# Kernel optimization log

Measured on AMD Instinct MI355X. Metric: run time of the kernel, lower is better.

Reference implementation:

```python
import jax, jax.numpy as jnp
import numpy as np

A0, A1, A2 = 1.0, 1.0, 0.5  # Taylor coefficients of exp around 0 (p=2)

B, H, N, D = 2, 16, 4096, 32


def setup_inputs() -> dict:
    key = jax.random.key(0)
    kq, kk, kv = jax.random.split(key, 3)
    q = jax.random.normal(kq, (B, H, N, D), dtype=jnp.float32)
    k = jax.random.normal(kk, (B, H, N, D), dtype=jnp.float32)
    v = jax.random.normal(kv, (B, H, N, D), dtype=jnp.float32)
    return {"q": q, "k": k, "v": v}


def reference(q, k, v):
    # fastmax_function with p=2, mask=False, normalize=False, dropout=0 -> temperature=1
    b, h, n, d = q.shape
    # quadratic feature maps: flatten of outer products, [b,h,n,d*d]
    q2 = (q[..., :, None] * q[..., None, :]).reshape(b, h, n, d * d)
    k2 = (k[..., :, None] * k[..., None, :]).reshape(b, h, n, d * d)
    # numerator: a0*sum(v) + a1*q(k^T v) + a2*q2(k2^T v)
    second_term = A1 * jnp.einsum('bhnd,bhne->bhde', k, v)           # [b,h,d,d]
    third_term = A2 * jnp.einsum('bhnf,bhne->bhfe', k2, v)           # [b,h,d^2,d]
    ans = (jnp.einsum('bhnd,bhde->bhne', q, second_term)
           + jnp.einsum('bhnf,bhfe->bhne', q2, third_term)
           + A0 * jnp.sum(v, axis=-2, keepdims=True))                 # [b,h,n,d]
    # denominator: a0*n + a1*q.sum(k) + a2*q2.sum(k2)
    div = (A0 * n
           + A1 * jnp.einsum('bhnd,bhd->bhn', q, jnp.sum(k, axis=-2))
           + A2 * jnp.einsum('bhnf,bhf->bhn', q2, jnp.sum(k2, axis=-2)))  # [b,h,n]
    return ans / div[..., None]
```

## Files before the change

kernel.cpp:

```cpp
#include <hip/hip_runtime.h>

#define NTOK 4096
#define NBH  32
#define NF   576
#define NE   33
#define NKT  18
#define GTF_BH (NKT * 3 * 64 * 8)
#define KC   16
#define NSTG 2
#define NVB  (KC * NBH)
#define NP8  (NBH * NE * NF / 8)

typedef _Float16 half_t;
typedef _Float16 half8 __attribute__((ext_vector_type(8)));
typedef _Float16 half4v __attribute__((ext_vector_type(4)));
typedef float f32x4 __attribute__((ext_vector_type(4)));

#define MFMA16(A,B,C) __builtin_amdgcn_mfma_f32_16x16x32_f16((A),(B),(C),0,0,0)

static __device__ __forceinline__ half8 splat8(half_t x) {
    return (half8){x, x, x, x, x, x, x, x};
}

static __device__ __forceinline__ int FS(int d) { return (d + (d >> 3)) & 15; }

__global__ __launch_bounds__(256, 2)
void ta_kernel(const float* __restrict__ kin, const float* __restrict__ vin,
               half_t* __restrict__ P)
{
    __shared__ __align__(16) half_t kb0[2 * 4096];
    __shared__ __align__(16) half_t vb0[2 * 4096];

    const int vb = blockIdx.x;
    const int bh = vb & (NBH - 1), kc = vb >> 5;
    const int t = threadIdx.x;
    const int w = t >> 6, lane = t & 63, l16 = lane & 15, quad = lane >> 4;
    const int pw = w * 144;
    const half8 h05 = splat8((half_t)0.5f);

    f32x4 acc[9][3];
    #pragma unroll
    for (int m = 0; m < 9; ++m)
        #pragma unroll
        for (int e = 0; e < 3; ++e)
            acc[m][e] = (f32x4){0.f, 0.f, 0.f, 0.f};

    int rotoff[9], rotsalt[9];
    #pragma unroll
    for (int mt = 0; mt < 9; ++mt) {
        const int pm = pw + mt * 16;
        int ro = 0, rs = 0;
        if (pm >= 32 && pm < 512) {
            const int s  = 1 + ((pm - 32) >> 5);
            const int i0 = (pm - 32) & 31;
            const int r  = (i0 + l16 + s) & 31;
            ro = r * 128;
            rs = FS(r);
        }
        rotoff[mt] = ro;
        rotsalt[mt] = rs;
    }
    const int sh0 = FS(l16), sh1 = FS(l16 + 16);

    const size_t fbase = ((size_t)bh * NTOK + kc * 256) * 32;
    const float4* k4 = (const float4*)kin + fbase / 4;
    const float4* v4 = (const float4*)vin + fbase / 4;

    float kaf[16], vaf[16];
    auto loadst = [&](int s) {
        const int base = s * 1024;
        #pragma unroll
        for (int r = 0; r < 4; ++r) {
            float4 kk = k4[base + t + 256 * r];
            float4 vv = v4[base + t + 256 * r];
            kaf[4*r+0] = kk.x; kaf[4*r+1] = kk.y; kaf[4*r+2] = kk.z; kaf[4*r+3] = kk.w;
            vaf[4*r+0] = vv.x; vaf[4*r+1] = vv.y; vaf[4*r+2] = vv.z; vaf[4*r+3] = vv.w;
        }
    };
    auto writest = [&](int buf) {
        half_t* kb = kb0 + buf * 4096;
        half_t* vb2 = vb0 + buf * 4096;
        #pragma unroll
        for (int r = 0; r < 4; ++r) {
            const int fi = t + 256 * r;
            const int n = fi >> 3, d4 = fi & 7;
            const int c = n >> 3, j = n & 7;
            #pragma unroll
            for (int i = 0; i < 4; ++i) {
                const int d = 4 * d4 + i;
                const int a = d * 128 + ((c ^ FS(d)) << 3) + j;
                kb[a] = (half_t)kaf[4*r+i];
                vb2[a] = (half_t)vaf[4*r+i];
            }
        }
    };
    auto compute = [&](int buf) {
        const half_t* kb = kb0 + buf * 4096;
        const half_t* vbp = vb0 + buf * 4096;
        #pragma unroll
        for (int kk = 0; kk < 4; ++kk) {
            const int c = kk * 4 + quad;
            half8 kj0 = *(const half8*)&kb[l16 * 128 + ((c ^ sh0) << 3)];
            half8 kj1 = *(const half8*)&kb[(l16 + 16) * 128 + ((c ^ sh1) << 3)];
            half8 bf0 = *(const half8*)&vbp[l16 * 128 + ((c ^ sh0) << 3)];
            half8 bf1 = *(const half8*)&vbp[(l16 + 16) * 128 + ((c ^ sh1) << 3)];
            half_t onec = (l16 == 0) ? (half_t)1 : (half_t)0;
            half8 bf2 = splat8(onec);
            #pragma unroll
            for (int mt = 0; mt < 9; ++mt) {
                const int pm = pw + mt * 16;
                half8 af;
                if (pm < 32) {
                    af = pm ? kj1 : kj0;
                } else if (pm < 512) {
                    half8 rot = *(const half8*)&kb[rotoff[mt] + ((c ^ rotsalt[mt]) << 3)];
                    af = (((pm - 32) & 16) ? kj1 : kj0) * rot;
                } else if (pm == 512) {
                    af = kj0 * kj1;
                } else if (pm == 528) {
                    af = (kj0 * h05) * kj0;
                } else if (pm == 544) {
                    af = (kj1 * h05) * kj1;
                } else {
                    af = bf2;
                }
                acc[mt][0] = MFMA16(af, bf0, acc[mt][0]);
                acc[mt][1] = MFMA16(af, bf1, acc[mt][1]);
                acc[mt][2] = MFMA16(af, bf2, acc[mt][2]);
            }
        }
    };

    loadst(0);
    writest(0);
    __syncthreads();
    for (int st = 0; st < NSTG; ++st) {
        const int cur = st & 1;
        if (st + 1 < NSTG) loadst(st + 1);
        compute(cur);
        if (st + 1 < NSTG) { writest(cur ^ 1); __syncthreads(); }
    }

    half_t* Pb = P + ((size_t)kc * NBH + bh) * NE * NF;
    #pragma unroll
    for (int mt = 0; mt < 9; ++mt) {
        int p0 = pw + mt * 16 + quad * 4;
        half4v h0 = {(half_t)acc[mt][0][0], (half_t)acc[mt][0][1],
                     (half_t)acc[mt][0][2], (half_t)acc[mt][0][3]};
        half4v h1 = {(half_t)acc[mt][1][0], (half_t)acc[mt][1][1],
                     (half_t)acc[mt][1][2], (half_t)acc[mt][1][3]};
        *(half4v*)&Pb[(size_t)l16 * NF + p0] = h0;
        *(half4v*)&Pb[(size_t)(l16 + 16) * NF + p0] = h1;
        if (l16 == 0) {
            half4v h2 = {(half_t)acc[mt][2][0], (half_t)acc[mt][2][1],
                         (half_t)acc[mt][2][2], (half_t)acc[mt][2][3]};
            *(half4v*)&Pb[(size_t)32 * NF + p0] = h2;
        }
    }
}

__global__ __launch_bounds__(256)
void ar_kernel(const half_t* __restrict__ P, half_t* __restrict__ GtF)
{
    const int idx = blockIdx.x * 256 + threadIdx.x;
    if (idx >= NP8) return;
    float s[8] = {0.f, 0.f, 0.f, 0.f, 0.f, 0.f, 0.f, 0.f};
    for (int c = 0; c < KC; ++c) {
        half8 h = *(const half8*)&P[(size_t)c * (NBH * NE * NF) + (size_t)idx * 8];
        #pragma unroll
        for (int j = 0; j < 8; ++j) s[j] += (float)h[j];
    }
    half8 o;
    #pragma unroll
    for (int j = 0; j < 8; ++j) o[j] = (half_t)s[j];
    int row = idx / 72;
    int p8 = idx - row * 72;
    int e = row % 33, bhh = row / 33;
    int kt = p8 >> 2, quad = p8 & 3;
    int rr = e >> 4, l16 = e & 15;
    size_t dst8 = (size_t)bhh * (GTF_BH / 8)
                + (size_t)(kt * 3 + rr) * 64 + quad * 16 + l16;
    *(half8*)&GtF[dst8 * 8] = o;
}

__global__ __launch_bounds__(256)
void b_kernel(const float* __restrict__ qin, const half_t* __restrict__ GtF,
              float* __restrict__ out)
{
    const int bh = blockIdx.x, mbq = blockIdx.y;
    const int t = threadIdx.x, w = t >> 6, lane = t & 63;
    const int l16 = lane & 15, quad = lane >> 4;
    __shared__ __align__(16) half_t qs2[256 * 56];
    __shared__ float denl[256];
    const size_t nbase = (size_t)bh * NTOK + mbq * 256;

    const float4* q4 = (const float4*)(qin + nbase * 32);
    #pragma unroll
    for (int r = 0; r < 8; ++r) {
        int f4 = t + 256 * r, n = f4 >> 3, d4 = f4 & 7;
        float4 vv = q4[f4];
        half4v h = {(half_t)vv.x, (half_t)vv.y, (half_t)vv.z, (half_t)vv.w};
        *(half4v*)&qs2[n * 56 + d4 * 4] = h;
        if (d4 < 4) *(half4v*)&qs2[n * 56 + 32 + d4 * 4] = h;
    }
    __syncthreads();

    const int rbase = w * 64;
    int tb[4];
    #pragma unroll
    for (int mt = 0; mt < 4; ++mt) tb[mt] = (rbase + mt * 16 + l16) * 56;

    half8 vq[4], hv[4], gv[4];
    #pragma unroll
    for (int mt = 0; mt < 4; ++mt) {
        const int qb = tb[mt] + quad * 8;
        vq[mt] = *(const half8*)&qs2[qb];
        hv[mt] = *(const half8*)&qs2[qb + 8];
        gv[mt] = *(const half8*)&qs2[qb + 16];
    }

    f32x4 acc[3][4];
    #pragma unroll
    for (int a = 0; a < 3; ++a)
        #pragma unroll
        for (int b = 0; b < 4; ++b)
            acc[a][b] = (f32x4){0.f, 0.f, 0.f, 0.f};

    const half_t* Gb = GtF + (size_t)bh * GTF_BH + (size_t)lane * 8;

#define LDF(kt, B) do { \
    _Pragma("unroll") \
    for (int rr = 0; rr < 3; ++rr) \
        (B)[rr] = *(const half8*)&Gb[(size_t)(((kt) * 3 + rr) * 64) * 8]; \
} while (0)

#define DO_MFMA(AF) do { \
    _Pragma("unroll") \
    for (int mt = 0; mt < 4; ++mt) { \
        acc[0][mt] = MFMA16((AF)[mt], B0[0], acc[0][mt]); \
        acc[1][mt] = MFMA16((AF)[mt], B0[1], acc[1][mt]); \
        acc[2][mt] = MFMA16((AF)[mt], B0[2], acc[2][mt]); \
    } \
} while (0)

#define RING() do { \
    _Pragma("unroll") \
    for (int rr = 0; rr < 3; ++rr) { B0[rr] = B1[rr]; B1[rr] = B2[rr]; B2[rr] = B3[rr]; } \
} while (0)

    half8 B0[3], B1[3], B2[3], B3[3];
    LDF(0, B0); LDF(1, B1); LDF(2, B2);

    {
        LDF(3, B3);
        DO_MFMA(vq);
        RING();
    }

#define QCHUNK(S) do { \
    if ((S) + 3 <= 17) LDF((S) + 3, B3); \
    half8 af[4]; \
    _Pragma("unroll") \
    for (int mt = 0; mt < 4; ++mt) { \
        half8 lo = ((S) < 8) ? vq[mt] : hv[mt]; \
        half8 hi = ((S) < 8) ? hv[mt] : gv[mt]; \
        half8 rot = __builtin_shufflevector(lo, hi, \
            ((S) & 7) + 0, ((S) & 7) + 1, ((S) & 7) + 2, ((S) & 7) + 3, \
            ((S) & 7) + 4, ((S) & 7) + 5, ((S) & 7) + 6, ((S) & 7) + 7); \
        af[mt] = vq[mt] * rot; \
    } \
    DO_MFMA(af); \
    RING(); \
} while (0)

    QCHUNK(1);  QCHUNK(2);  QCHUNK(3);  QCHUNK(4);  QCHUNK(5);
    QCHUNK(6);  QCHUNK(7);  QCHUNK(8);  QCHUNK(9);  QCHUNK(10);
    QCHUNK(11); QCHUNK(12); QCHUNK(13); QCHUNK(14); QCHUNK(15);

    {
        half8 af[4];
        #pragma unroll
        for (int mt = 0; mt < 4; ++mt) {
            const int off = tb[mt] + ((quad >= 2) ? (quad - 2) : quad) * 8;
            half8 Ld = *(const half8*)&qs2[off];
            af[mt] = (quad < 2) ? (vq[mt] * gv[mt]) : (Ld * Ld);
        }
        DO_MFMA(af);
        RING();
    }
    {
        const half8 zero = {};
        half8 c10 = {};
        c10[0] = (half_t)1;
        half8 af[4];
        #pragma unroll
        for (int mt = 0; mt < 4; ++mt) {
            half8 d = gv[mt] * gv[mt];
            af[mt] = (quad < 2) ? d : ((quad == 2) ? c10 : zero);
        }
        DO_MFMA(af);
    }
#undef QCHUNK
#undef RING
#undef DO_MFMA
#undef LDF

    if (l16 == 0) {
        #pragma unroll
        for (int mt = 0; mt < 4; ++mt)
            #pragma unroll
            for (int r = 0; r < 4; ++r)
                denl[rbase + mt * 16 + quad * 4 + r] = acc[2][mt][r];
    }
    __syncthreads();
    #pragma unroll
    for (int mt = 0; mt < 4; ++mt) {
        float inv[4];
        #pragma unroll
        for (int r = 0; r < 4; ++r)
            inv[r] = __builtin_amdgcn_rcpf(denl[rbase + mt * 16 + quad * 4 + r]);
        #pragma unroll
        for (int r = 0; r < 4; ++r) {
            size_t ro = (nbase + rbase + mt * 16 + quad * 4 + r) * 32;
            out[ro + l16] = acc[0][mt][r] * inv[r];
            out[ro + l16 + 16] = acc[1][mt][r] * inv[r];
        }
    }
}

extern "C" void kernel_launch(void* const* d_in, const int* in_sizes, int n_in,
                              void* d_out, int out_size, void* d_ws, size_t ws_size,
                              hipStream_t stream)
{
    const float* q = (const float*)d_in[0];
    const float* k = (const float*)d_in[1];
    const float* v = (const float*)d_in[2];
    float* out = (float*)d_out;

    const size_t planeHalves = (size_t)NBH * NE * NF;
    half_t* P = (half_t*)d_ws;
    half_t* GtF = P + (size_t)KC * planeHalves;

    ta_kernel<<<dim3(NVB), 256, 0, stream>>>(k, v, P);
    ar_kernel<<<dim3((NP8 + 255) / 256), 256, 0, stream>>>(P, GtF);
    b_kernel<<<dim3(NBH, 16), 256, 0, stream>>>(q, GtF, out);
}
```

Before: 123.1 us.

## Replace split-K partial buffer and reduction kernel with fp32 atomics into G

The ta_kernel now accumulates its per-chunk partial products directly into an fp32 G buffer in the b_kernel layout using unsafeAtomicAdd, after a memset. This removes the separate ar_kernel and the fp16 partial plane round trip. b_kernel loads fp32 values and converts them to fp16 on the fly. In exchange it issues many scalar atomics (16-way contention per element), doubles the G read size in b_kernel, and adds a memset launch.

```diff
diff --git a/kernel.cpp b/kernel.cpp
--- a/kernel.cpp
+++ b/kernel.cpp
@@ -9,11 +9,9 @@
 #define KC   16
 #define NSTG 2
 #define NVB  (KC * NBH)
-#define NP8  (NBH * NE * NF / 8)
 
 typedef _Float16 half_t;
 typedef _Float16 half8 __attribute__((ext_vector_type(8)));
-typedef _Float16 half4v __attribute__((ext_vector_type(4)));
 typedef float f32x4 __attribute__((ext_vector_type(4)));
 
 #define MFMA16(A,B,C) __builtin_amdgcn_mfma_f32_16x16x32_f16((A),(B),(C),0,0,0)
@@ -26,7 +24,7 @@
 
 __global__ __launch_bounds__(256, 2)
 void ta_kernel(const float* __restrict__ kin, const float* __restrict__ vin,
-               half_t* __restrict__ P)
+               float* __restrict__ G32)
 {
     __shared__ __align__(16) half_t kb0[2 * 4096];
     __shared__ __align__(16) half_t vb0[2 * 4096];
@@ -141,50 +139,35 @@
         if (st + 1 < NSTG) { writest(cur ^ 1); __syncthreads(); }
     }
 
-    half_t* Pb = P + ((size_t)kc * NBH + bh) * NE * NF;
+    float* Gb = G32 + (size_t)bh * GTF_BH;
     #pragma unroll
     for (int mt = 0; mt < 9; ++mt) {
-        int p0 = pw + mt * 16 + quad * 4;
-        half4v h0 = {(half_t)acc[mt][0][0], (half_t)acc[mt][0][1],
-                     (half_t)acc[mt][0][2], (half_t)acc[mt][0][3]};
-        half4v h1 = {(half_t)acc[mt][1][0], (half_t)acc[mt][1][1],
-                     (half_t)acc[mt][1][2], (half_t)acc[mt][1][3]};
-        *(half4v*)&Pb[(size_t)l16 * NF + p0] = h0;
-        *(half4v*)&Pb[(size_t)(l16 + 16) * NF + p0] = h1;
+        #pragma unroll
+        for (int et = 0; et < 2; ++et) {
+            #pragma unroll
+            for (int r = 0; r < 4; ++r) {
+                const int p = pw + mt * 16 + quad * 4 + r;
+                if (p > 560) continue;
+                const int kt = p >> 5, qb = (p >> 3) & 3, j = p & 7;
+                const int off = (((kt * 3 + et) * 64) + qb * 16 + l16) * 8 + j;
+                unsafeAtomicAdd(&Gb[off], acc[mt][et][r]);
+            }
+        }
         if (l16 == 0) {
-            half4v h2 = {(half_t)acc[mt][2][0], (half_t)acc[mt][2][1],
-                         (half_t)acc[mt][2][2], (half_t)acc[mt][2][3]};
-            *(half4v*)&Pb[(size_t)32 * NF + p0] = h2;
+            #pragma unroll
+            for (int r = 0; r < 4; ++r) {
+                const int p = pw + mt * 16 + quad * 4 + r;
+                if (p > 560) continue;
+                const int kt = p >> 5, qb = (p >> 3) & 3, j = p & 7;
+                const int off = (((kt * 3 + 2) * 64) + qb * 16) * 8 + j;
+                unsafeAtomicAdd(&Gb[off], acc[mt][2][r]);
+            }
         }
     }
 }
 
 __global__ __launch_bounds__(256)
-void ar_kernel(const half_t* __restrict__ P, half_t* __restrict__ GtF)
-{
-    const int idx = blockIdx.x * 256 + threadIdx.x;
-    if (idx >= NP8) return;
-    float s[8] = {0.f, 0.f, 0.f, 0.f, 0.f, 0.f, 0.f, 0.f};
-    for (int c = 0; c < KC; ++c) {
-        half8 h = *(const half8*)&P[(size_t)c * (NBH * NE * NF) + (size_t)idx * 8];
-        #pragma unroll
-        for (int j = 0; j < 8; ++j) s[j] += (float)h[j];
-    }
-    half8 o;
-    #pragma unroll
-    for (int j = 0; j < 8; ++j) o[j] = (half_t)s[j];
-    int row = idx / 72;
-    int p8 = idx - row * 72;
-    int e = row % 33, bhh = row / 33;
-    int kt = p8 >> 2, quad = p8 & 3;
-    int rr = e >> 4, l16 = e & 15;
-    size_t dst8 = (size_t)bhh * (GTF_BH / 8)
-                + (size_t)(kt * 3 + rr) * 64 + quad * 16 + l16;
-    *(half8*)&GtF[dst8 * 8] = o;
-}
-
-__global__ __launch_bounds__(256)
-void b_kernel(const float* __restrict__ qin, const half_t* __restrict__ GtF,
+void b_kernel(const float* __restrict__ qin, const float* __restrict__ G32,
               float* __restrict__ out)
 {
     const int bh = blockIdx.x, mbq = blockIdx.y;
@@ -199,9 +182,14 @@
     for (int r = 0; r < 8; ++r) {
         int f4 = t + 256 * r, n = f4 >> 3, d4 = f4 & 7;
         float4 vv = q4[f4];
-        half4v h = {(half_t)vv.x, (half_t)vv.y, (half_t)vv.z, (half_t)vv.w};
-        *(half4v*)&qs2[n * 56 + d4 * 4] = h;
-        if (d4 < 4) *(half4v*)&qs2[n * 56 + 32 + d4 * 4] = h;
+        half_t h0 = (half_t)vv.x, h1 = (half_t)vv.y;
+        half_t h2 = (half_t)vv.z, h3 = (half_t)vv.w;
+        half_t* row = &qs2[n * 56 + d4 * 4];
+        row[0] = h0; row[1] = h1; row[2] = h2; row[3] = h3;
+        if (d4 < 4) {
+            half_t* row2 = &qs2[n * 56 + 32 + d4 * 4];
+            row2[0] = h0; row2[1] = h1; row2[2] = h2; row2[3] = h3;
+        }
     }
     __syncthreads();
 
@@ -226,12 +214,18 @@
         for (int b = 0; b < 4; ++b)
             acc[a][b] = (f32x4){0.f, 0.f, 0.f, 0.f};
 
-    const half_t* Gb = GtF + (size_t)bh * GTF_BH + (size_t)lane * 8;
+    const float* Gb = G32 + (size_t)bh * GTF_BH + (size_t)lane * 8;
 
 #define LDF(kt, B) do { \
     _Pragma("unroll") \
-    for (int rr = 0; rr < 3; ++rr) \
-        (B)[rr] = *(const half8*)&Gb[(size_t)(((kt) * 3 + rr) * 64) * 8]; \
+    for (int rr = 0; rr < 3; ++rr) { \
+        const float* src = &Gb[(size_t)(((kt) * 3 + rr) * 64) * 8]; \
+        f32x4 lo = *(const f32x4*)src; \
+        f32x4 hi = *(const f32x4*)(src + 4); \
+        half8 hb = {(half_t)lo[0], (half_t)lo[1], (half_t)lo[2], (half_t)lo[3], \
+                    (half_t)hi[0], (half_t)hi[1], (half_t)hi[2], (half_t)hi[3]}; \
+        (B)[rr] = hb; \
+    } \
 } while (0)
 
 #define DO_MFMA(AF) do { \
@@ -337,11 +331,9 @@
     const float* v = (const float*)d_in[2];
     float* out = (float*)d_out;
 
-    const size_t planeHalves = (size_t)NBH * NE * NF;
-    half_t* P = (half_t*)d_ws;
-    half_t* GtF = P + (size_t)KC * planeHalves;
-
-    ta_kernel<<<dim3(NVB), 256, 0, stream>>>(k, v, P);
-    ar_kernel<<<dim3((NP8 + 255) / 256), 256, 0, stream>>>(P, GtF);
-    b_kernel<<<dim3(NBH, 16), 256, 0, stream>>>(q, GtF, out);
+    float* G32 = (float*)d_ws;
+
+    hipMemsetAsync(G32, 0, (size_t)NBH * GTF_BH * sizeof(float), stream);
+    ta_kernel<<<dim3(NVB), 256, 0, stream>>>(k, v, G32);
+    b_kernel<<<dim3(NBH, 16), 256, 0, stream>>>(q, G32, out);
 }
```

After: 254.3 us. 2.07x slower.

## Stage G matrix into LDS via async global_load_lds in two halves

Applied to the files above, without the earlier changes.

In b_kernel, the G factor tiles were loaded straight from global memory into registers through a four-deep register ring. They are now copied into shared memory with async global-to-LDS loads, in two phases of nine k-tiles each, and every MFMA step reads its B operand from LDS. This is meant to cut global memory traffic, since all four waves shared the same G data, and to free the ring's registers. In exchange it adds about 27KB of LDS per block, which may lower occupancy. It also adds barriers mid-loop, and the second-phase load is exposed with no overlap. The first stage does overlap with the q conversion.

```diff
diff --git a/kernel.cpp b/kernel.cpp
--- a/kernel.cpp
+++ b/kernel.cpp
@@ -6,6 +6,7 @@
 #define NE   33
 #define NKT  18
 #define GTF_BH (NKT * 3 * 64 * 8)
+#define GTF_HALF (9 * 3 * 64 * 8)
 #define KC   16
 #define NSTG 2
 #define NVB  (KC * NBH)
@@ -15,8 +16,14 @@
 typedef _Float16 half8 __attribute__((ext_vector_type(8)));
 typedef _Float16 half4v __attribute__((ext_vector_type(4)));
 typedef float f32x4 __attribute__((ext_vector_type(4)));
+typedef unsigned int u32;
 
 #define MFMA16(A,B,C) __builtin_amdgcn_mfma_f32_16x16x32_f16((A),(B),(C),0,0,0)
+
+#define ASYNC_CP16(dst_lds, src_glb) \
+    __builtin_amdgcn_global_load_lds( \
+        (const __attribute__((address_space(1))) u32*)(const void*)(src_glb), \
+        (__attribute__((address_space(3))) u32*)(void*)(dst_lds), 16, 0, 0)
 
 static __device__ __forceinline__ half8 splat8(half_t x) {
     return (half8){x, x, x, x, x, x, x, x};
@@ -191,8 +198,21 @@
     const int t = threadIdx.x, w = t >> 6, lane = t & 63;
     const int l16 = lane & 15, quad = lane >> 4;
     __shared__ __align__(16) half_t qs2[256 * 56];
+    __shared__ __align__(16) half_t gs[GTF_HALF];
     __shared__ float denl[256];
     const size_t nbase = (size_t)bh * NTOK + mbq * 256;
+
+    const half_t* Gsrc = GtF + (size_t)bh * GTF_BH + (size_t)lane * 8;
+    auto stage = [&](int phase) {
+        const half_t* src = Gsrc + phase * GTF_HALF;
+        #pragma unroll
+        for (int i = 0; i < 7; ++i) {
+            const int c = w + 4 * i;
+            if (c < 27)
+                ASYNC_CP16(gs + c * 512, src + c * 512);
+        }
+    };
+    stage(0);
 
     const float4* q4 = (const float4*)(qin + nbase * 32);
     #pragma unroll
@@ -226,39 +246,24 @@
         for (int b = 0; b < 4; ++b)
             acc[a][b] = (f32x4){0.f, 0.f, 0.f, 0.f};
 
-    const half_t* Gb = GtF + (size_t)bh * GTF_BH + (size_t)lane * 8;
-
-#define LDF(kt, B) do { \
+#define LDB(ktL, B) do { \
     _Pragma("unroll") \
     for (int rr = 0; rr < 3; ++rr) \
-        (B)[rr] = *(const half8*)&Gb[(size_t)(((kt) * 3 + rr) * 64) * 8]; \
+        (B)[rr] = *(const half8*)&gs[(((ktL) * 3 + rr) * 64 + lane) * 8]; \
 } while (0)
 
-#define DO_MFMA(AF) do { \
+#define DO_MFMA(AF, B) do { \
     _Pragma("unroll") \
     for (int mt = 0; mt < 4; ++mt) { \
-        acc[0][mt] = MFMA16((AF)[mt], B0[0], acc[0][mt]); \
-        acc[1][mt] = MFMA16((AF)[mt], B0[1], acc[1][mt]); \
-        acc[2][mt] = MFMA16((AF)[mt], B0[2], acc[2][mt]); \
+        acc[0][mt] = MFMA16((AF)[mt], (B)[0], acc[0][mt]); \
+        acc[1][mt] = MFMA16((AF)[mt], (B)[1], acc[1][mt]); \
+        acc[2][mt] = MFMA16((AF)[mt], (B)[2], acc[2][mt]); \
     } \
 } while (0)
 
-#define RING() do { \
-    _Pragma("unroll") \
-    for (int rr = 0; rr < 3; ++rr) { B0[rr] = B1[rr]; B1[rr] = B2[rr]; B2[rr] = B3[rr]; } \
-} while (0)
-
-    half8 B0[3], B1[3], B2[3], B3[3];
-    LDF(0, B0); LDF(1, B1); LDF(2, B2);
-
-    {
-        LDF(3, B3);
-        DO_MFMA(vq);
-        RING();
-    }
-
-#define QCHUNK(S) do { \
-    if ((S) + 3 <= 17) LDF((S) + 3, B3); \
+#define QCHUNK(S, KTL) do { \
+    half8 Bc[3]; \
+    LDB((KTL), Bc); \
     half8 af[4]; \
     _Pragma("unroll") \
     for (int mt = 0; mt < 4; ++mt) { \
@@ -269,15 +274,27 @@
             ((S) & 7) + 4, ((S) & 7) + 5, ((S) & 7) + 6, ((S) & 7) + 7); \
         af[mt] = vq[mt] * rot; \
     } \
-    DO_MFMA(af); \
-    RING(); \
+    DO_MFMA(af, Bc); \
 } while (0)
 
-    QCHUNK(1);  QCHUNK(2);  QCHUNK(3);  QCHUNK(4);  QCHUNK(5);
-    QCHUNK(6);  QCHUNK(7);  QCHUNK(8);  QCHUNK(9);  QCHUNK(10);
-    QCHUNK(11); QCHUNK(12); QCHUNK(13); QCHUNK(14); QCHUNK(15);
-
     {
+        half8 Bc[3];
+        LDB(0, Bc);
+        DO_MFMA(vq, Bc);
+    }
+    QCHUNK(1, 1);  QCHUNK(2, 2);  QCHUNK(3, 3);  QCHUNK(4, 4);
+    QCHUNK(5, 5);  QCHUNK(6, 6);  QCHUNK(7, 7);  QCHUNK(8, 8);
+
+    __syncthreads();
+    stage(1);
+    __syncthreads();
+
+    QCHUNK(9, 0);  QCHUNK(10, 1); QCHUNK(11, 2); QCHUNK(12, 3);
+    QCHUNK(13, 4); QCHUNK(14, 5); QCHUNK(15, 6);
+
+    {
+        half8 Bc[3];
+        LDB(7, Bc);
         half8 af[4];
         #pragma unroll
         for (int mt = 0; mt < 4; ++mt) {
@@ -285,10 +302,11 @@
             half8 Ld = *(const half8*)&qs2[off];
             af[mt] = (quad < 2) ? (vq[mt] * gv[mt]) : (Ld * Ld);
         }
-        DO_MFMA(af);
-        RING();
+        DO_MFMA(af, Bc);
     }
     {
+        half8 Bc[3];
+        LDB(8, Bc);
         const half8 zero = {};
         half8 c10 = {};
         c10[0] = (half_t)1;
@@ -298,12 +316,11 @@
             half8 d = gv[mt] * gv[mt];
             af[mt] = (quad < 2) ? d : ((quad == 2) ? c10 : zero);
         }
-        DO_MFMA(af);
+        DO_MFMA(af, Bc);
     }
 #undef QCHUNK
-#undef RING
 #undef DO_MFMA
-#undef LDF
+#undef LDB
 
     if (l16 == 0) {
         #pragma unroll
```

After: 124.3 us, median of 2. Within noise of the previous version (+1.0%).
